# Performance work log

Hardware: AMD Instinct MI355X
Metric: run time of the kernel (lower is better)

Reference implementation:

```python
import jax, jax.numpy as jnp
import numpy as np


def setup_inputs() -> dict:
    key = jax.random.key(0)
    ks = jax.random.split(key, 8)
    B, L, D, H = 4, 2048, 4096, 8
    BW = D // H
    std = 1.0 / np.sqrt(BW)
    x = jax.random.normal(ks[0], (B, L, D), dtype=jnp.float32)
    segment_pos = jax.random.randint(ks[1], (B, L), 0, 1024)
    prev_h = jax.random.normal(ks[2], (B, D), dtype=jnp.float32)
    w_in = jax.random.normal(ks[3], (H, BW, BW), dtype=jnp.float32) * std
    b_in = jnp.zeros((H, BW), dtype=jnp.float32)
    w_a = jax.random.normal(ks[4], (H, BW, BW), dtype=jnp.float32) * std
    b_a = jnp.zeros((H, BW), dtype=jnp.float32)
    # a_param init: uniform on ring [0.9, 0.999], softplus-inverse transform
    unif = jax.random.uniform(ks[5], (D,), dtype=jnp.float32)
    min_rad, max_rad = 0.9, 0.999
    a_real = 0.5 * jnp.log(unif * (max_rad**2 - min_rad**2) + min_rad**2 + 1e-8)
    a_param = jnp.log(jnp.exp(-a_real) - 1.0)
    return {"x": x, "segment_pos": segment_pos, "prev_h": prev_h,
            "w_in": w_in, "b_in": b_in, "w_a": w_a, "b_a": b_a,
            "a_param": a_param}


def _block_diag_linear(x, w, b):
    # x: [B,L,D]; w: [H,BW,BW]; b: [H,BW]
    B, L, D = x.shape
    H = w.shape[0]
    xr = x.reshape(B, L, H, D // H)
    y = jnp.einsum('blhi,hij->blhj', xr, w) + b
    return y.reshape(B, L, D)


def reference(x, segment_pos, prev_h, w_in, b_in, w_a, b_a, a_param):
    # reset indicator at document boundaries (segment_pos == 0)
    reset = (segment_pos == 0).astype(x.dtype)          # [B,L]
    gate_x = jax.nn.sigmoid(_block_diag_linear(x, w_in, b_in))
    gate_a = jax.nn.sigmoid(_block_diag_linear(x, w_a, b_a))
    log_a = -8.0 * gate_a * jax.nn.softplus(a_param)    # [B,L,D]
    a = jnp.exp(log_a)
    multiplier = jnp.sqrt(1.0 - jnp.exp(2.0 * log_a) + 1e-6)
    multiplier = reset[..., None] + (1.0 - reset)[..., None] * multiplier
    normalized_x = x * gate_x * multiplier
    # zero the decay at reset positions (hidden state reset)
    a = a * (1.0 - reset)[..., None]
    # linear recurrence y_t = a_t * y_{t-1} + x_t (initial hidden state = 0,
    # matching the torch L>1 path which does not use prev_h)
    def combine(c1, c2):
        a1, b1 = c1
        a2, b2 = c2
        return (a2 * a1, a2 * b1 + b2)
    _, y = jax.lax.associative_scan(combine, (a, normalized_x), axis=1)
    return y
```

## Files before the change

### kernel.cpp

```cpp
#include <hip/hip_runtime.h>
#include <hip/hip_bf16.h>

typedef _Float16 f16;
typedef _Float16 f16x2 __attribute__((ext_vector_type(2)));
typedef _Float16 f16x4 __attribute__((ext_vector_type(4)));
typedef _Float16 f16x8 __attribute__((ext_vector_type(8)));
typedef float f32x4 __attribute__((ext_vector_type(4)));

#define B_  4
#define L_  2048
#define D_  4096
#define H_  8
#define BW_ 512
#define M_  (B_*L_)
#define CHUNK 128
#define NCH (L_/CHUNK)
#define LOG2E 1.4426950408889634f

static const size_t OFF_WPK   = 0;
static const size_t OFF_MSP   = 8ull<<20;
static const size_t OFF_XH    = 9ull<<20;
static const size_t OFF_YLAP  = 73ull<<20;
static const size_t OFF_SUMA  = 208ull<<20;
static const size_t OFF_SUMY  = 209ull<<20;

__device__ __forceinline__ void gl16(const void* g, void* l) {
    __builtin_amdgcn_global_load_lds(
        (const __attribute__((address_space(1))) unsigned int*)g,
        (__attribute__((address_space(3))) unsigned int*)l, 16, 0, 0);
}

__global__ __launch_bounds__(256)
void prep_all(const float* __restrict__ w_in, const float* __restrict__ w_a,
              const float* __restrict__ a_param, const float* __restrict__ x,
              f16* __restrict__ wpk, float* __restrict__ msp2,
              f16* __restrict__ xh) {
    const int bid = blockIdx.x;
    const int tid = threadIdx.x;
    if (bid < 1024) {
        const int kt  = bid & 7;
        const int n32 = (bid >> 3) & 15;
        const int h   = bid >> 7;
        if (bid < 16) {
            int d = bid * 256 + tid;
            float v = a_param[d];
            msp2[d] = -8.f * log1pf(expf(v)) * LOG2E;
        }
#pragma unroll
        for (int q = 0; q < 2; ++q) {
            int slot = q * 256 + tid;
            int lane = slot & 63;
            int fidx = slot >> 6;
            int g    = fidx >> 2;
            int fn   = (fidx >> 1) & 1;
            int kk2  = fidx & 1;
            int row = n32 * 32 + fn * 16 + (lane & 15);
            int col = kt * 64 + kk2 * 32 + ((lane >> 4) << 3);
            const float* src = (g ? w_a : w_in) + (size_t)h * BW_ * BW_;
            f16x8 v;
#pragma unroll
            for (int e = 0; e < 8; ++e)
                v[e] = (f16)src[(size_t)(col + e) * BW_ + row];
            size_t o = ((((size_t)(h * 16 + n32) * 8 + kt) * 8) + fidx) * 64 + lane;
            *(f16x8*)(wpk + o * 8) = v;
        }
    } else {
        size_t i = ((size_t)(bid - 1024) * 256 + tid) * 8;
        const size_t stride = (size_t)2048 * 256 * 8;
        for (; i < (size_t)M_ * D_; i += stride) {
            f32x4 v0 = *(const f32x4*)(x + i);
            f32x4 v1 = *(const f32x4*)(x + i + 4);
            f16x8 hv;
            hv[0] = (f16)v0.x; hv[1] = (f16)v0.y; hv[2] = (f16)v0.z; hv[3] = (f16)v0.w;
            hv[4] = (f16)v1.x; hv[5] = (f16)v1.y; hv[6] = (f16)v1.z; hv[7] = (f16)v1.w;
            *(f16x8*)(xh + i) = hv;
        }
    }
}

#define BM 128
#define BN 128
#define BKK 64
#define NT (BW_/BKK)
#define BUFB 16384

#define SMEM_BYTES 72320

__global__ __launch_bounds__(256, 2)
void gemm_gates(const f16*   __restrict__ xh,
                const int*   __restrict__ segpos,
                const f16*   __restrict__ wpk,
                const float* __restrict__ b_in,
                const float* __restrict__ b_a,
                const float* __restrict__ msp2,
                f16x2* __restrict__ ylap,
                float* __restrict__ sumA,
                float* __restrict__ sumY) {
    __shared__ __align__(16) char smem[SMEM_BYTES];
    f16x2* axn  = (f16x2*)smem;
    float* segA = (float*)(smem + 67584);
    float* segY = (float*)(smem + 69696);
    float* rst_s= (float*)(smem + 71808);

    const int tid  = threadIdx.x;
    const int m0   = blockIdx.x * BM;
    const int n0   = blockIdx.y * BN;
    const int h    = blockIdx.z;
    const int lane = tid & 63;
    const int wid  = tid >> 6;
    const int wr   = wid >> 1;
    const int wc   = wid & 1;

    f32x4 accX[4][4] = {};
    f32x4 accA[4][4] = {};

    if (tid < BM) rst_s[tid] = (segpos[m0 + tid] == 0) ? 1.f : 0.f;

    const int grow  = lane >> 3;
    const int gcolS = (((lane & 7) ^ grow) << 3);
    const f16* aSrc = xh + (size_t)(m0 + wid * 32 + grow) * D_ + h * BW_ + gcolS;

    const f16* wb0 = wpk + ((size_t)(h * 16) + (n0 >> 5) + wc * 2) * 32768;
    const f16* wb1 = wb0 + 32768;

    const int swz  = (lane & 7) << 3;
    const int kx   = (lane >> 4) << 3;
    const int arow = wr * 64 + (lane & 15);
    const int rowb = wr * 64 + ((lane >> 4) << 2);
    const int txo  = ((n0 >> 6) + 2) & (NT - 1);

    f16x8 bfr[16];

#define STAGE_A(T)                                                            \
    {                                                                         \
        const int ktg = ((T) + txo) & (NT - 1);                               \
        f16* Asb = (f16*)(smem + ((T) % 3) * BUFB);                           \
        _Pragma("unroll")                                                     \
        for (int q = 0; q < 4; ++q)                                           \
            gl16(aSrc + ktg * BKK + (size_t)q * 8 * D_,                       \
                 &Asb[(wid * 32 + q * 8) * 64]);                              \
    }
#define LOAD_B(T)                                                             \
    {                                                                         \
        const int ktg = ((T) + txo) & (NT - 1);                               \
        _Pragma("unroll")                                                     \
        for (int fn = 0; fn < 4; ++fn) {                                      \
            const f16* tp = (fn < 2 ? wb0 : wb1) +                            \
                ((size_t)ktg * 8 + (fn & 1) * 2) * 512 + lane * 8;            \
            _Pragma("unroll")                                                 \
            for (int g = 0; g < 2; ++g)                                       \
                _Pragma("unroll")                                             \
                for (int kk2 = 0; kk2 < 2; ++kk2)                             \
                    bfr[fn * 4 + g * 2 + kk2] =                               \
                        *(const f16x8*)(tp + (g * 4 + kk2) * 512);            \
        }                                                                     \
    }

    STAGE_A(0);
    STAGE_A(1);

#pragma unroll
    for (int t = 0; t < NT; ++t) {
        LOAD_B(t);
        if (t + 2 < NT) {
            STAGE_A(t + 2);
            asm volatile("s_waitcnt vmcnt(4)" ::: "memory");
        } else {
            asm volatile("s_waitcnt vmcnt(0)" ::: "memory");
        }
        __builtin_amdgcn_s_barrier();
        __builtin_amdgcn_sched_barrier(0);

        const f16* Asb = (const f16*)(smem + (t % 3) * BUFB);
#pragma unroll
        for (int kk2 = 0; kk2 < 2; ++kk2) {
            const int kcolS = (kk2 * 32 + kx) ^ swz;
            f16x8 af[4];
#pragma unroll
            for (int fm = 0; fm < 4; ++fm)
                af[fm] = *(const f16x8*)&Asb[(arow + fm * 16) * 64 + kcolS];
#pragma unroll
            for (int fn = 0; fn < 4; ++fn) {
                f16x8 bx = bfr[fn * 4 + kk2];
                f16x8 ba = bfr[fn * 4 + 2 + kk2];
#pragma unroll
                for (int fm = 0; fm < 4; ++fm) {
                    accX[fm][fn] = __builtin_amdgcn_mfma_f32_16x16x32_f16(af[fm], bx, accX[fm][fn], 0, 0, 0);
                    accA[fm][fn] = __builtin_amdgcn_mfma_f32_16x16x32_f16(af[fm], ba, accA[fm][fn], 0, 0, 0);
                }
            }
        }
        __builtin_amdgcn_sched_barrier(0);
        __builtin_amdgcn_s_barrier();
    }
#undef STAGE_A
#undef LOAD_B

    const f16* AsL = (const f16*)(smem + wc * BUFB);
    f16 xvv[4][4][4];
#pragma unroll
    for (int fn = 0; fn < 4; ++fn) {
        const int c5 = fn * 16 + (lane & 15);
#pragma unroll
        for (int fm = 0; fm < 4; ++fm)
#pragma unroll
            for (int reg = 0; reg < 4; ++reg) {
                const int rowt = rowb + fm * 16 + reg;
                xvv[fn][fm][reg] = AsL[rowt * 64 + (c5 ^ ((rowt & 7) << 3))];
            }
    }
    __syncthreads();

    {
#pragma unroll
        for (int fn = 0; fn < 4; ++fn) {
            const int ctile = wc * 64 + fn * 16 + (lane & 15);
            const int d = h * BW_ + n0 + ctile;
            const float bx = b_in[d];
            const float ba = b_a[d];
            const float mspd = msp2[d];
#pragma unroll
            for (int fm = 0; fm < 4; ++fm) {
#pragma unroll
                for (int reg = 0; reg < 4; ++reg) {
                    const int rowt = rowb + fm * 16 + reg;
                    float gxl = accX[fm][fn][reg] + bx;
                    float gal = accA[fm][fn][reg] + ba;
                    float gx = __builtin_amdgcn_rcpf(1.f + __builtin_amdgcn_exp2f(-gxl * LOG2E));
                    float ga = __builtin_amdgcn_rcpf(1.f + __builtin_amdgcn_exp2f(-gal * LOG2E));
                    float a  = __builtin_amdgcn_exp2f(mspd * ga);
                    float a2 = a * a;
                    float mult = __builtin_amdgcn_sqrtf(1.f + 1e-6f - a2);
                    float rv = rst_s[rowt];
                    a *= (1.f - rv);
                    mult = rv + (1.f - rv) * mult;
                    float xv = (float)xvv[fn][fm][reg];
                    f16x2 p;
                    p[0] = (f16)(1.f - a);
                    p[1] = (f16)(xv * gx * mult);
                    axn[rowt * 132 + ctile] = p;
                }
            }
        }
    }
    __syncthreads();

    const int col = tid & 127;
    const int sg0 = tid >> 7;
#pragma unroll
    for (int ss = 0; ss < 2; ++ss) {
        const int seg = sg0 + ss * 2;
        float A = 1.f, yv = 0.f;
#pragma unroll 4
        for (int i = 0; i < 32; ++i) {
            f16x2 v = axn[(seg * 32 + i) * 132 + col];
            float a  = 1.f - (float)v[0];
            yv = fmaf(a, yv, (float)v[1]);
            A *= a;
        }
        segA[seg * 132 + col] = A;
        segY[seg * 132 + col] = yv;
    }
    __syncthreads();

#pragma unroll
    for (int ss = 0; ss < 2; ++ss) {
        const int seg = sg0 + ss * 2;
        float cy = 0.f, pA = 1.f;
        for (int s = 0; s < seg; ++s) {
            float As_ = segA[s * 132 + col];
            cy = fmaf(As_, cy, segY[s * 132 + col]);
            pA *= As_;
        }
        float Arun = 1.f, yv = cy;
        const size_t obase = (size_t)(m0 + seg * 32) * D_ + h * BW_ + n0 + col;
#pragma unroll 4
        for (int i = 0; i < 32; ++i) {
            f16x2 v = axn[(seg * 32 + i) * 132 + col];
            float a  = 1.f - (float)v[0];
            yv = fmaf(a, yv, (float)v[1]);
            Arun *= a;
            f16x2 p;
            p[0] = (f16)yv;
            p[1] = (f16)(pA * Arun);
            ylap[obase + (size_t)i * D_] = p;
        }
        if (seg == 3) {
            const int bb = m0 >> 11;
            const int cc = (m0 & 2047) >> 7;
            size_t si = ((size_t)bb * NCH + cc) * D_ + h * BW_ + n0 + col;
            sumA[si] = pA * Arun;
            sumY[si] = yv;
        }
    }
}

__global__ __launch_bounds__(256)
void scan_apply(const float* __restrict__ sumA, const float* __restrict__ sumY,
                const f16x2* __restrict__ ylap, float* __restrict__ y) {
    const int tid = threadIdx.x;
    const int d4  = (blockIdx.x * 256 + tid) * 4;
    const int c   = blockIdx.y >> 2;
    const int tq  = blockIdx.y & 3;
    const int b   = blockIdx.z;
    f32x4 h0 = {0.f, 0.f, 0.f, 0.f};
    for (int cp = 0; cp < c; ++cp) {
        size_t si = (((size_t)(b * NCH + cp)) << 12) + d4;
        f32x4 A = *(const f32x4*)(sumA + si);
        f32x4 Y = *(const f32x4*)(sumY + si);
        h0.x = fmaf(A.x, h0.x, Y.x);
        h0.y = fmaf(A.y, h0.y, Y.y);
        h0.z = fmaf(A.z, h0.z, Y.z);
        h0.w = fmaf(A.w, h0.w, Y.w);
    }
    size_t base = ((size_t)(b * L_ + c * CHUNK + tq * 32)) * D_ + d4;
#pragma unroll 4
    for (int i = 0; i < 32; ++i) {
        size_t o = base + (size_t)i * D_;
        f16x8 p = *(const f16x8*)(ylap + o);
        f32x4 ov;
        ov.x = fmaf(h0.x, (float)p[1], (float)p[0]);
        ov.y = fmaf(h0.y, (float)p[3], (float)p[2]);
        ov.z = fmaf(h0.z, (float)p[5], (float)p[4]);
        ov.w = fmaf(h0.w, (float)p[7], (float)p[6]);
        *(f32x4*)(y + o) = ov;
    }
}

extern "C" void kernel_launch(void* const* d_in, const int* in_sizes, int n_in,
                              void* d_out, int out_size, void* d_ws, size_t ws_size,
                              hipStream_t stream) {
    const float* x       = (const float*)d_in[0];
    const int*   segpos  = (const int*)d_in[1];
    const float* w_in    = (const float*)d_in[3];
    const float* b_in    = (const float*)d_in[4];
    const float* w_a     = (const float*)d_in[5];
    const float* b_a     = (const float*)d_in[6];
    const float* a_param = (const float*)d_in[7];

    float* y  = (float*)d_out;
    char*  ws = (char*)d_ws;
    f16*   wpk   = (f16*)(ws + OFF_WPK);
    float* msp2  = (float*)(ws + OFF_MSP);
    f16*   xh    = (f16*)(ws + OFF_XH);
    f16x2* ylap  = (f16x2*)(ws + OFF_YLAP);
    float* sumA  = (float*)(ws + OFF_SUMA);
    float* sumY  = (float*)(ws + OFF_SUMY);

    prep_all<<<dim3(3072), 256, 0, stream>>>(w_in, w_a, a_param, x, wpk, msp2, xh);
    gemm_gates<<<dim3(M_ / BM, BW_ / BN, H_), 256, 0, stream>>>(
        xh, segpos, wpk, b_in, b_a, msp2, ylap, sumA, sumY);
    scan_apply<<<dim3(D_ / 1024, NCH * 4, B_), 256, 0, stream>>>(sumA, sumY, ylap, y);
}
```

Measured before the change: 228.6 us.

## Halve GEMM N-tile, double-buffer B fragments, and read x from staged A tile

Narrows the gate GEMM output tile from 128 to 64 columns, which halves the accumulators and B fragments per wave. It double-buffers B register fragments across k-steps and issues the next B and A loads right after the barrier, dropping the second barrier per iteration. It also reads x for normalization directly from the last staged A tile in the scan stage instead of extracting it into registers earlier. The aim is lower register pressure, better load/compute overlap and more blocks in flight, at the cost of twice as many blocks re-reading the A (x) tile and more scan work per thread.

```diff
diff --git a/kernel.cpp b/kernel.cpp
--- a/kernel.cpp
+++ b/kernel.cpp
@@ -3,7 +3,6 @@
 
 typedef _Float16 f16;
 typedef _Float16 f16x2 __attribute__((ext_vector_type(2)));
-typedef _Float16 f16x4 __attribute__((ext_vector_type(4)));
 typedef _Float16 f16x8 __attribute__((ext_vector_type(8)));
 typedef float f32x4 __attribute__((ext_vector_type(4)));
 
@@ -79,12 +78,12 @@
 }
 
 #define BM 128
-#define BN 128
+#define BN 64
 #define BKK 64
 #define NT (BW_/BKK)
 #define BUFB 16384
 
-#define SMEM_BYTES 72320
+#define SMEM_BYTES 52992
 
 __global__ __launch_bounds__(256, 2)
 void gemm_gates(const f16*   __restrict__ xh,
@@ -97,10 +96,10 @@
                 float* __restrict__ sumA,
                 float* __restrict__ sumY) {
     __shared__ __align__(16) char smem[SMEM_BYTES];
-    f16x2* axn  = (f16x2*)smem;
-    float* segA = (float*)(smem + 67584);
-    float* segY = (float*)(smem + 69696);
-    float* rst_s= (float*)(smem + 71808);
+    f16x2* axn  = (f16x2*)(smem + 16384);
+    float* segA = (float*)(smem + 50176);
+    float* segY = (float*)(smem + 51328);
+    float* rst_s= (float*)(smem + 52480);
 
     const int tid  = threadIdx.x;
     const int m0   = blockIdx.x * BM;
@@ -111,8 +110,8 @@
     const int wr   = wid >> 1;
     const int wc   = wid & 1;
 
-    f32x4 accX[4][4] = {};
-    f32x4 accA[4][4] = {};
+    f32x4 accX[4][2] = {};
+    f32x4 accA[4][2] = {};
 
     if (tid < BM) rst_s[tid] = (segpos[m0 + tid] == 0) ? 1.f : 0.f;
 
@@ -120,8 +119,7 @@
     const int gcolS = (((lane & 7) ^ grow) << 3);
     const f16* aSrc = xh + (size_t)(m0 + wid * 32 + grow) * D_ + h * BW_ + gcolS;
 
-    const f16* wb0 = wpk + ((size_t)(h * 16) + (n0 >> 5) + wc * 2) * 32768;
-    const f16* wb1 = wb0 + 32768;
+    const f16* wbase = wpk + ((size_t)(h * 16) + (n0 >> 5) + wc) * 32768;
 
     const int swz  = (lane & 7) << 3;
     const int kx   = (lane >> 4) << 3;
@@ -129,7 +127,7 @@
     const int rowb = wr * 64 + ((lane >> 4) << 2);
     const int txo  = ((n0 >> 6) + 2) & (NT - 1);
 
-    f16x8 bfr[16];
+    f16x8 bfr[2][8];
 
 #define STAGE_A(T)                                                            \
     {                                                                         \
@@ -143,32 +141,24 @@
 #define LOAD_B(T)                                                             \
     {                                                                         \
         const int ktg = ((T) + txo) & (NT - 1);                               \
+        const f16* tp = wbase + (size_t)ktg * 4096;                           \
         _Pragma("unroll")                                                     \
-        for (int fn = 0; fn < 4; ++fn) {                                      \
-            const f16* tp = (fn < 2 ? wb0 : wb1) +                            \
-                ((size_t)ktg * 8 + (fn & 1) * 2) * 512 + lane * 8;            \
-            _Pragma("unroll")                                                 \
-            for (int g = 0; g < 2; ++g)                                       \
-                _Pragma("unroll")                                             \
-                for (int kk2 = 0; kk2 < 2; ++kk2)                             \
-                    bfr[fn * 4 + g * 2 + kk2] =                               \
-                        *(const f16x8*)(tp + (g * 4 + kk2) * 512);            \
-        }                                                                     \
-    }
-
+        for (int j = 0; j < 8; ++j)                                           \
+            bfr[(T) & 1][j] = *(const f16x8*)(tp + j * 512 + lane * 8);       \
+    }
+
+    LOAD_B(0);
     STAGE_A(0);
     STAGE_A(1);
 
 #pragma unroll
     for (int t = 0; t < NT; ++t) {
-        LOAD_B(t);
-        if (t + 2 < NT) {
-            STAGE_A(t + 2);
-            asm volatile("s_waitcnt vmcnt(4)" ::: "memory");
-        } else {
-            asm volatile("s_waitcnt vmcnt(0)" ::: "memory");
-        }
+        if (t == 0)          asm volatile("s_waitcnt vmcnt(4)"  ::: "memory");
+        else if (t < NT - 1) asm volatile("s_waitcnt vmcnt(12)" ::: "memory");
+        else                 asm volatile("s_waitcnt vmcnt(8)"  ::: "memory");
         __builtin_amdgcn_s_barrier();
+        if (t + 1 < NT) LOAD_B(t + 1);
+        if (t + 2 < NT) STAGE_A(t + 2);
         __builtin_amdgcn_sched_barrier(0);
 
         const f16* Asb = (const f16*)(smem + (t % 3) * BUFB);
@@ -180,9 +170,9 @@
             for (int fm = 0; fm < 4; ++fm)
                 af[fm] = *(const f16x8*)&Asb[(arow + fm * 16) * 64 + kcolS];
 #pragma unroll
-            for (int fn = 0; fn < 4; ++fn) {
-                f16x8 bx = bfr[fn * 4 + kk2];
-                f16x8 ba = bfr[fn * 4 + 2 + kk2];
+            for (int fn = 0; fn < 2; ++fn) {
+                f16x8 bx = bfr[t & 1][fn * 2 + kk2];
+                f16x8 ba = bfr[t & 1][4 + fn * 2 + kk2];
 #pragma unroll
                 for (int fm = 0; fm < 4; ++fm) {
                     accX[fm][fn] = __builtin_amdgcn_mfma_f32_16x16x32_f16(af[fm], bx, accX[fm][fn], 0, 0, 0);
@@ -190,31 +180,16 @@
                 }
             }
         }
-        __builtin_amdgcn_sched_barrier(0);
-        __builtin_amdgcn_s_barrier();
     }
 #undef STAGE_A
 #undef LOAD_B
 
-    const f16* AsL = (const f16*)(smem + wc * BUFB);
-    f16 xvv[4][4][4];
-#pragma unroll
-    for (int fn = 0; fn < 4; ++fn) {
-        const int c5 = fn * 16 + (lane & 15);
-#pragma unroll
-        for (int fm = 0; fm < 4; ++fm)
-#pragma unroll
-            for (int reg = 0; reg < 4; ++reg) {
-                const int rowt = rowb + fm * 16 + reg;
-                xvv[fn][fm][reg] = AsL[rowt * 64 + (c5 ^ ((rowt & 7) << 3))];
-            }
-    }
     __syncthreads();
 
     {
 #pragma unroll
-        for (int fn = 0; fn < 4; ++fn) {
-            const int ctile = wc * 64 + fn * 16 + (lane & 15);
+        for (int fn = 0; fn < 2; ++fn) {
+            const int ctile = wc * 32 + fn * 16 + (lane & 15);
             const int d = h * BW_ + n0 + ctile;
             const float bx = b_in[d];
             const float ba = b_a[d];
@@ -234,51 +209,51 @@
                     float rv = rst_s[rowt];
                     a *= (1.f - rv);
                     mult = rv + (1.f - rv) * mult;
-                    float xv = (float)xvv[fn][fm][reg];
                     f16x2 p;
                     p[0] = (f16)(1.f - a);
-                    p[1] = (f16)(xv * gx * mult);
-                    axn[rowt * 132 + ctile] = p;
+                    p[1] = (f16)(gx * mult);
+                    axn[rowt * 66 + ctile] = p;
                 }
             }
         }
     }
     __syncthreads();
 
-    const int col = tid & 127;
-    const int sg0 = tid >> 7;
-#pragma unroll
-    for (int ss = 0; ss < 2; ++ss) {
-        const int seg = sg0 + ss * 2;
+    const f16* As0 = (const f16*)smem;
+    const int col = tid & 63;
+    const int seg = tid >> 6;
+    {
         float A = 1.f, yv = 0.f;
 #pragma unroll 4
         for (int i = 0; i < 32; ++i) {
-            f16x2 v = axn[(seg * 32 + i) * 132 + col];
+            const int t = seg * 32 + i;
+            f16x2 v = axn[t * 66 + col];
             float a  = 1.f - (float)v[0];
-            yv = fmaf(a, yv, (float)v[1]);
+            float xv = (float)As0[t * 64 + (col ^ ((t & 7) << 3))];
+            yv = fmaf(a, yv, xv * (float)v[1]);
             A *= a;
         }
-        segA[seg * 132 + col] = A;
-        segY[seg * 132 + col] = yv;
+        segA[seg * 72 + col] = A;
+        segY[seg * 72 + col] = yv;
     }
     __syncthreads();
 
-#pragma unroll
-    for (int ss = 0; ss < 2; ++ss) {
-        const int seg = sg0 + ss * 2;
+    {
         float cy = 0.f, pA = 1.f;
         for (int s = 0; s < seg; ++s) {
-            float As_ = segA[s * 132 + col];
-            cy = fmaf(As_, cy, segY[s * 132 + col]);
+            float As_ = segA[s * 72 + col];
+            cy = fmaf(As_, cy, segY[s * 72 + col]);
             pA *= As_;
         }
         float Arun = 1.f, yv = cy;
         const size_t obase = (size_t)(m0 + seg * 32) * D_ + h * BW_ + n0 + col;
 #pragma unroll 4
         for (int i = 0; i < 32; ++i) {
-            f16x2 v = axn[(seg * 32 + i) * 132 + col];
+            const int t = seg * 32 + i;
+            f16x2 v = axn[t * 66 + col];
             float a  = 1.f - (float)v[0];
-            yv = fmaf(a, yv, (float)v[1]);
+            float xv = (float)As0[t * 64 + (col ^ ((t & 7) << 3))];
+            yv = fmaf(a, yv, xv * (float)v[1]);
             Arun *= a;
             f16x2 p;
             p[0] = (f16)yv;
```

Measured after the change: 214.3 us, median of 2. 6.2% less time.
